# Kernel optimization log

Hardware: AMD Instinct MI355X
Metric: run time of the kernel (lower is better)

Reference implementation:

```python
import jax, jax.numpy as jnp
import numpy as np

B, N, C = 16, 2048, 384
CLUSTER_NUM = 512
K_NN = 5


def setup_inputs() -> dict:
    key = jax.random.key(0)
    k1, k2, k3, k4 = jax.random.split(key, 4)
    x = jax.random.normal(k1, (B, N, C), dtype=jnp.float32)
    idx_token = jax.random.randint(k2, (B, N), 0, N)
    agg_weight = jnp.ones((B, N, 1), dtype=jnp.float32)
    density_noise = jax.random.uniform(k3, (B, N), dtype=jnp.float32)
    score_w = jax.random.normal(k4, (1, C), dtype=jnp.float32) * 0.02
    score_b = jnp.zeros((1,), dtype=jnp.float32)
    return {"x": x, "idx_token": idx_token, "agg_weight": agg_weight,
            "density_noise": density_noise, "score_w": score_w, "score_b": score_b}


def _cluster_dpc_knn(x, density_noise, cluster_num, k):
    # x: [B,N,C]; clustering is done under no_grad in the original
    x = jax.lax.stop_gradient(x)
    b, n, c = x.shape
    sq = jnp.sum(x * x, axis=-1)  # [B,N]
    d2 = sq[:, :, None] + sq[:, None, :] - 2.0 * jnp.einsum('bnc,bmc->bnm', x, x)
    dist = jnp.sqrt(jnp.maximum(d2, 0.0)) / (c ** 0.5)  # [B,N,N] cdist/sqrt(C)
    # k smallest distances per row
    neg_near, _ = jax.lax.top_k(-dist, k)                # [B,N,k]
    density = jnp.exp(-jnp.mean(neg_near * neg_near, axis=-1))  # [B,N]
    density = density + density_noise * 1e-6             # tie-break noise
    mask = (density[:, None, :] > density[:, :, None]).astype(x.dtype)  # [B,N,N]
    dist_max = jnp.max(dist.reshape(b, -1), axis=-1)[:, None, None]
    dmin = jnp.min(dist * mask + dist_max * (1.0 - mask), axis=-1)  # [B,N]
    score = dmin * density
    _, index_down = jax.lax.top_k(score, cluster_num)    # [B,K] cluster centers
    dist_sub = jnp.take_along_axis(dist, index_down[:, :, None], axis=1)  # [B,K,N]
    idx_cluster = jnp.argmin(dist_sub, axis=1)           # [B,N]
    bi = jnp.arange(b)[:, None]
    centers = jnp.broadcast_to(jnp.arange(cluster_num)[None, :], (b, cluster_num))
    idx_cluster = idx_cluster.at[bi, index_down].set(centers)
    return idx_cluster, index_down


def reference(x, idx_token, agg_weight, density_noise, score_w, score_b):
    b, n, c = x.shape
    kc = CLUSTER_NUM
    # token score -> weight (equal_weight=False)
    token_weight = jnp.exp(x @ score_w.T + score_b)      # [B,N,1]
    idx_cluster, _ = _cluster_dpc_knn(x, density_noise, kc, K_NN)
    # merge tokens via segment sums
    bi = jnp.arange(b)[:, None]
    idx = (idx_cluster + bi * kc).reshape(-1)            # [B*N]
    all_weight = jax.ops.segment_sum(token_weight.reshape(-1, 1), idx,
                                     num_segments=b * kc) + 1e-6  # [B*K,1]
    norm_weight = token_weight / all_weight[idx].reshape(b, n, 1)
    x_merged = jax.ops.segment_sum((x * norm_weight).reshape(-1, c), idx,
                                   num_segments=b * kc).reshape(b, kc, c)
    idx_token_new = jnp.take_along_axis(idx_cluster, idx_token, axis=1)  # [B,N]
    weight_t = jnp.take_along_axis(norm_weight, idx_token[:, :, None], axis=1)
    agg_weight_new = agg_weight * weight_t               # [B,N,1]
    return x_merged, idx_token_new, agg_weight_new
```

## Files before the change

### kernel.cpp

```cpp
#include <hip/hip_runtime.h>
#include <math.h>

static constexpr int BB  = 16;
static constexpr int NN  = 2048;
static constexpr int CC  = 384;
static constexpr int KCL = 512;
static constexpr float RSQC = 0.051031036307982884f;

typedef short  bf16x8 __attribute__((ext_vector_type(8)));
typedef float  f32x4  __attribute__((ext_vector_type(4)));

__device__ __forceinline__ unsigned short f2b(float v) {
    unsigned u = __float_as_uint(v);
    unsigned r = (u + 0x7FFFu + ((u >> 16) & 1u)) >> 16;
    return (unsigned short)r;
}
__device__ __forceinline__ float b2f(unsigned short b) {
    return __uint_as_float(((unsigned)b) << 16);
}
__device__ __forceinline__ void gload16(const void* g, void* l) {
    __builtin_amdgcn_global_load_lds(
        (const __attribute__((address_space(1))) void*)g,
        (__attribute__((address_space(3))) void*)l, 16, 0, 0);
}
__device__ __forceinline__ void ins5(float* t5, float v) {
    if (v < t5[4]) {
        t5[4] = v;
        #pragma unroll
        for (int q = 4; q > 0; --q) {
            if (t5[q] < t5[q - 1]) { float tmp = t5[q - 1]; t5[q - 1] = t5[q]; t5[q] = tmp; }
        }
    }
}

__global__ __launch_bounds__(256) void k_prep(
    const float* __restrict__ x, const float* __restrict__ sw,
    const float* __restrict__ sb, float* __restrict__ sq, float* __restrict__ tw,
    unsigned short* __restrict__ Xh, unsigned short* __restrict__ Xl)
{
    int row  = blockIdx.x * 4 + (threadIdx.x >> 6);
    int lane = threadIdx.x & 63;
    const float* xr = x + (size_t)row * CC;
    unsigned short* xh = Xh + (size_t)row * CC;
    unsigned short* xl = Xl + (size_t)row * CC;
    float s2 = 0.f, sd = 0.f;
    for (int c = lane; c < CC; c += 64) {
        float v = xr[c];
        s2 += v * v;
        sd += v * sw[c];
        unsigned short h = f2b(v);
        xh[c] = h;
        xl[c] = f2b(v - b2f(h));
    }
    #pragma unroll
    for (int o = 32; o > 0; o >>= 1) {
        s2 += __shfl_down(s2, o);
        sd += __shfl_down(sd, o);
    }
    if (lane == 0) {
        sq[row] = s2;
        tw[row] = expf(sd + sb[0]);
    }
}

__global__ __launch_bounds__(256) void k_rowstats(
    const float* __restrict__ x, const float* __restrict__ sw,
    const float* __restrict__ sb, float* __restrict__ sq, float* __restrict__ tw)
{
    int row  = blockIdx.x * 4 + (threadIdx.x >> 6);
    int lane = threadIdx.x & 63;
    const float* xr = x + (size_t)row * CC;
    float s2 = 0.f, sd = 0.f;
    for (int c = lane; c < CC; c += 64) {
        float v = xr[c];
        s2 += v * v;
        sd += v * sw[c];
    }
    #pragma unroll
    for (int o = 32; o > 0; o >>= 1) {
        s2 += __shfl_down(s2, o);
        sd += __shfl_down(sd, o);
    }
    if (lane == 0) {
        sq[row] = s2;
        tw[row] = expf(sd + sb[0]);
    }
}


__global__ __launch_bounds__(256) void k_gemm_sym(
    const unsigned short* __restrict__ Xh, const unsigned short* __restrict__ Xl,
    const float* __restrict__ sq, float* __restrict__ D, int b0)
{
    const int b = b0 + blockIdx.z;
    int q = blockIdx.x;
    int ti = 0;
    while (q >= (16 - ti)) { q -= (16 - ti); ++ti; }
    const int tj = ti + q;
    const int i0 = ti * 128, j0 = tj * 128;

    const unsigned short* Xhb = Xh + (size_t)b * NN * CC;
    const unsigned short* Xlb = Xl + (size_t)b * NN * CC;
    const float* sqb = sq + b * NN;
    float* Db = D + (size_t)blockIdx.z * NN * NN;

    __shared__ union {
        unsigned short u16[4][128][32];
        float tr[64][129];
    } sm;

    const int t  = threadIdx.x;
    const int w  = t >> 6;
    const int l  = t & 63;
    const int wr = w >> 1, wc = w & 1;
    const int lt = l & 15, sl = l >> 4;

    f32x4 acc[4][4];
    #pragma unroll
    for (int fr = 0; fr < 4; ++fr)
        #pragma unroll
        for (int fc = 0; fc < 4; ++fc) acc[fr][fc] = (f32x4)0.0f;

    for (int kc = 0; kc < CC; kc += 32) {
        #pragma unroll
        for (int p = 0; p < 4; ++p) {
            const unsigned short* src = (p == 0) ? Xhb : (p == 1) ? Xlb
                                      : (p == 2) ? Xhb : Xlb;
            const int base0 = (p < 2) ? i0 : j0;
            #pragma unroll
            for (int u = 0; u < 2; ++u) {
                int seg = w * 2 + u;
                int r   = seg * 16 + (l >> 2);
                int s   = (l & 3) ^ ((r >> 1) & 3);
                gload16(src + (size_t)(base0 + r) * CC + kc + s * 8,
                        &sm.u16[p][seg * 16][0]);
            }
        }
        __syncthreads();

        bf16x8 fah[4], fal[4], fbh[4], fbl[4];
        #pragma unroll
        for (int fr = 0; fr < 4; ++fr) {
            int ra = wr * 64 + fr * 16 + lt;
            int sa = (sl ^ ((ra >> 1) & 3)) * 8;
            fah[fr] = *(const bf16x8*)&sm.u16[0][ra][sa];
            fal[fr] = *(const bf16x8*)&sm.u16[1][ra][sa];
        }
        #pragma unroll
        for (int fc = 0; fc < 4; ++fc) {
            int rb = wc * 64 + fc * 16 + lt;
            int sb_ = (sl ^ ((rb >> 1) & 3)) * 8;
            fbh[fc] = *(const bf16x8*)&sm.u16[2][rb][sb_];
            fbl[fc] = *(const bf16x8*)&sm.u16[3][rb][sb_];
        }
        #pragma unroll
        for (int fr = 0; fr < 4; ++fr)
            #pragma unroll
            for (int fc = 0; fc < 4; ++fc) {
                acc[fr][fc] = __builtin_amdgcn_mfma_f32_16x16x32_bf16(
                    fah[fr], fbh[fc], acc[fr][fc], 0, 0, 0);
                acc[fr][fc] = __builtin_amdgcn_mfma_f32_16x16x32_bf16(
                    fah[fr], fbl[fc], acc[fr][fc], 0, 0, 0);
                acc[fr][fc] = __builtin_amdgcn_mfma_f32_16x16x32_bf16(
                    fal[fr], fbh[fc], acc[fr][fc], 0, 0, 0);
            }
        __syncthreads();
    }

    float sqr[4][4], sqc[4];
    #pragma unroll
    for (int fr = 0; fr < 4; ++fr)
        #pragma unroll
        for (int reg = 0; reg < 4; ++reg)
            sqr[fr][reg] = sqb[i0 + wr * 64 + fr * 16 + sl * 4 + reg];
    #pragma unroll
    for (int fc = 0; fc < 4; ++fc)
        sqc[fc] = sqb[j0 + wc * 64 + fc * 16 + lt];

    #pragma unroll
    for (int fr = 0; fr < 4; ++fr)
        #pragma unroll
        for (int fc = 0; fc < 4; ++fc)
            #pragma unroll
            for (int reg = 0; reg < 4; ++reg) {
                int row = i0 + wr * 64 + fr * 16 + sl * 4 + reg;
                int col = j0 + wc * 64 + fc * 16 + lt;
                float d2 = fmaxf(sqr[fr][reg] + sqc[fc] - 2.0f * acc[fr][fc][reg], 0.0f);
                Db[(size_t)row * NN + col] = d2;
            }

    if (ti != tj) {
        #pragma unroll
        for (int h = 0; h < 2; ++h) {
            __syncthreads();
            if (wr == h) {
                #pragma unroll
                for (int fr = 0; fr < 4; ++fr)
                    #pragma unroll
                    for (int fc = 0; fc < 4; ++fc)
                        #pragma unroll
                        for (int reg = 0; reg < 4; ++reg) {
                            int rl = fr * 16 + sl * 4 + reg;
                            int cl = wc * 64 + fc * 16 + lt;
                            float d2 = fmaxf(sqr[fr][reg] + sqc[fc]
                                             - 2.0f * acc[fr][fc][reg], 0.0f);
                            sm.tr[rl][cl] = d2;
                        }
            }
            __syncthreads();
            for (int idx = t; idx < 128 * 64; idx += 256) {
                int c  = idx >> 6;
                int rl = idx & 63;
                Db[(size_t)(j0 + c) * NN + i0 + h * 64 + rl] = sm.tr[rl][c];
            }
        }
    }
}

__global__ __launch_bounds__(256) void k_density2(
    const float* __restrict__ D, const float* __restrict__ noise,
    float* __restrict__ dens, float* __restrict__ rowmax)
{
    int gid  = blockIdx.x * 4 + (threadIdx.x >> 6);
    int lane = threadIdx.x & 63;
    const float* row = D + (size_t)gid * NN;
    float t5[5] = {1e30f, 1e30f, 1e30f, 1e30f, 1e30f};
    float mx = 0.f;
    #pragma unroll
    for (int it = 0; it < 8; ++it) {
        float4 v = ((const float4*)row)[it * 64 + lane];
        mx = fmaxf(mx, fmaxf(fmaxf(v.x, v.y), fmaxf(v.z, v.w)));
        ins5(t5, v.x); ins5(t5, v.y); ins5(t5, v.z); ins5(t5, v.w);
    }
    #pragma unroll
    for (int o = 1; o < 64; o <<= 1) {
        float b0 = __shfl_xor(t5[0], o), b1 = __shfl_xor(t5[1], o);
        float b2 = __shfl_xor(t5[2], o), b3 = __shfl_xor(t5[3], o);
        float b4 = __shfl_xor(t5[4], o);
        mx = fmaxf(mx, __shfl_xor(mx, o));
        ins5(t5, b0); ins5(t5, b1); ins5(t5, b2); ins5(t5, b3); ins5(t5, b4);
    }
    if (lane == 0) {
        float m2 = (t5[0] + t5[1] + t5[2] + t5[3] + t5[4]) * (1.0f / (5.0f * CC));
        dens[gid]   = expf(-m2) + noise[gid] * 1e-6f;
        rowmax[gid] = mx;
    }
}

__global__ __launch_bounds__(256) void k_distmax2(
    const float* __restrict__ rowmax, float* __restrict__ dmax)
{
    int b = blockIdx.x, t = threadIdx.x;
    float m = 0.f;
    for (int i = t; i < NN; i += 256) m = fmaxf(m, rowmax[b * NN + i]);
    __shared__ float red[256];
    red[t] = m; __syncthreads();
    for (int o = 128; o > 0; o >>= 1) {
        if (t < o) red[t] = fmaxf(red[t], red[t + o]);
        __syncthreads();
    }
    if (t == 0) dmax[b] = sqrtf(red[0]) * RSQC;
}

__global__ __launch_bounds__(256) void k_dmin2(
    const float* __restrict__ D, const float* __restrict__ dens,
    const float* __restrict__ dmax, float* __restrict__ score)
{
    int gid  = blockIdx.x * 4 + (threadIdx.x >> 6);
    int lane = threadIdx.x & 63;
    int bl   = gid >> 11;
    const float* row = D + (size_t)gid * NN;
    const float* dn  = dens + (size_t)bl * NN;
    float di = dens[gid];
    float m = 1e30f;
    #pragma unroll
    for (int it = 0; it < 8; ++it) {
        float4 v  = ((const float4*)row)[it * 64 + lane];
        float4 dj = ((const float4*)dn)[it * 64 + lane];
        if (dj.x > di) m = fminf(m, v.x);
        if (dj.y > di) m = fminf(m, v.y);
        if (dj.z > di) m = fminf(m, v.z);
        if (dj.w > di) m = fminf(m, v.w);
    }
    #pragma unroll
    for (int o = 32; o > 0; o >>= 1) m = fminf(m, __shfl_down(m, o));
    if (lane == 0) {
        float dm = fminf(sqrtf(m) * RSQC, dmax[bl]);
        score[gid] = dm * di;
    }
}

__global__ __launch_bounds__(256) void k_assign2(
    const float* __restrict__ D, const int* __restrict__ idown,
    const int* __restrict__ invc, int* __restrict__ idxc)
{
    int bl = blockIdx.y;
    int tl = threadIdx.x & 63;
    int g  = threadIdx.x >> 6;
    int n  = blockIdx.x * 64 + tl;
    const float* Db = D + (size_t)bl * NN * NN;
    const int* idb  = idown + bl * KCL;
    float best = 1e30f; int bk = 0;
    for (int k = g * 128; k < (g + 1) * 128; ++k) {
        float v = Db[(size_t)idb[k] * NN + n];
        if (v < best) { best = v; bk = k; }
    }
    __shared__ float bvs[4][64];
    __shared__ int   bks[4][64];
    bvs[g][tl] = best; bks[g][tl] = bk;
    __syncthreads();
    if (threadIdx.x < 64) {
        float bv = bvs[0][threadIdx.x]; int bkk = bks[0][threadIdx.x];
        #pragma unroll
        for (int gg = 1; gg < 4; ++gg) {
            if (bvs[gg][threadIdx.x] < bv) { bv = bvs[gg][threadIdx.x]; bkk = bks[gg][threadIdx.x]; }
        }
        int nn = blockIdx.x * 64 + threadIdx.x;
        int iv = invc[bl * NN + nn];
        idxc[bl * NN + nn] = (iv >= 0) ? iv : bkk;
    }
}


__global__ __launch_bounds__(256) void k_density(
    const float* __restrict__ x, const float* __restrict__ sq,
    const float* __restrict__ noise, float* __restrict__ dens,
    float* __restrict__ rowmax)
{
    const int b  = blockIdx.y;
    const int i0 = blockIdx.x * 64;
    const float* xb  = x + (size_t)b * NN * CC;
    const float* sqb = sq + b * NN;
    __shared__ float As[16][64];
    __shared__ float Bs[16][64];
    __shared__ float mrg[64][16][5];
    __shared__ float mrgmax[64][16];
    const int t  = threadIdx.x;
    const int tx = t & 15, ty = t >> 4;
    const int lr = t >> 2, lk4 = (t & 3) * 4;

    float top[4][5];
    float rmax[4];
    float sqi[4];
    #pragma unroll
    for (int r = 0; r < 4; ++r) {
        sqi[r]  = sqb[i0 + ty * 4 + r];
        rmax[r] = 0.f;
        #pragma unroll
        for (int q = 0; q < 5; ++q) top[r][q] = 1e30f;
    }

    for (int j0 = 0; j0 < NN; j0 += 64) {
        float acc[4][4];
        #pragma unroll
        for (int r = 0; r < 4; ++r)
            #pragma unroll
            for (int s = 0; s < 4; ++s) acc[r][s] = 0.f;

        for (int k0 = 0; k0 < CC; k0 += 16) {
            float4 av = *(const float4*)(xb + (size_t)(i0 + lr) * CC + k0 + lk4);
            float4 bv = *(const float4*)(xb + (size_t)(j0 + lr) * CC + k0 + lk4);
            As[lk4 + 0][lr] = av.x; As[lk4 + 1][lr] = av.y;
            As[lk4 + 2][lr] = av.z; As[lk4 + 3][lr] = av.w;
            Bs[lk4 + 0][lr] = bv.x; Bs[lk4 + 1][lr] = bv.y;
            Bs[lk4 + 2][lr] = bv.z; Bs[lk4 + 3][lr] = bv.w;
            __syncthreads();
            #pragma unroll
            for (int kk = 0; kk < 16; ++kk) {
                float4 a4 = *(const float4*)&As[kk][ty * 4];
                float4 b4 = *(const float4*)&Bs[kk][tx * 4];
                float ar[4] = {a4.x, a4.y, a4.z, a4.w};
                float br[4] = {b4.x, b4.y, b4.z, b4.w};
                #pragma unroll
                for (int r = 0; r < 4; ++r)
                    #pragma unroll
                    for (int s = 0; s < 4; ++s)
                        acc[r][s] = fmaf(ar[r], br[s], acc[r][s]);
            }
            __syncthreads();
        }
        float sqj[4];
        #pragma unroll
        for (int s = 0; s < 4; ++s) sqj[s] = sqb[j0 + tx * 4 + s];
        #pragma unroll
        for (int r = 0; r < 4; ++r) {
            #pragma unroll
            for (int s = 0; s < 4; ++s) {
                float d2 = sqi[r] + sqj[s] - 2.0f * acc[r][s];
                float d  = sqrtf(fmaxf(d2, 0.0f)) * RSQC;
                rmax[r] = fmaxf(rmax[r], d);
                if (d < top[r][4]) {
                    top[r][4] = d;
                    #pragma unroll
                    for (int q = 4; q > 0; --q) {
                        if (top[r][q] < top[r][q - 1]) {
                            float tmp = top[r][q - 1];
                            top[r][q - 1] = top[r][q];
                            top[r][q] = tmp;
                        }
                    }
                }
            }
        }
    }
    #pragma unroll
    for (int r = 0; r < 4; ++r) {
        #pragma unroll
        for (int q = 0; q < 5; ++q) mrg[ty * 4 + r][tx][q] = top[r][q];
        mrgmax[ty * 4 + r][tx] = rmax[r];
    }
    __syncthreads();
    if (t < 64) {
        float t5[5] = {1e30f, 1e30f, 1e30f, 1e30f, 1e30f};
        float mx = 0.f;
        for (int c = 0; c < 16; ++c) {
            mx = fmaxf(mx, mrgmax[t][c]);
            #pragma unroll
            for (int q = 0; q < 5; ++q) ins5(t5, mrg[t][c][q]);
        }
        float m2 = (t5[0]*t5[0] + t5[1]*t5[1] + t5[2]*t5[2] +
                    t5[3]*t5[3] + t5[4]*t5[4]) / 5.0f;
        int i = i0 + t;
        dens[b * NN + i]   = expf(-m2) + noise[b * NN + i] * 1e-6f;
        rowmax[b * NN + i] = mx;
    }
}

__global__ __launch_bounds__(256) void k_distmax(
    const float* __restrict__ rowmax, float* __restrict__ dmax)
{
    int b = blockIdx.x, t = threadIdx.x;
    float m = 0.f;
    for (int i = t; i < NN; i += 256) m = fmaxf(m, rowmax[b * NN + i]);
    __shared__ float red[256];
    red[t] = m; __syncthreads();
    for (int o = 128; o > 0; o >>= 1) {
        if (t < o) red[t] = fmaxf(red[t], red[t + o]);
        __syncthreads();
    }
    if (t == 0) dmax[b] = red[0];
}

__global__ __launch_bounds__(256) void k_dmin(
    const float* __restrict__ x, const float* __restrict__ sq,
    const float* __restrict__ dens, const float* __restrict__ dmax,
    float* __restrict__ score)
{
    const int b  = blockIdx.y;
    const int i0 = blockIdx.x * 64;
    const float* xb  = x + (size_t)b * NN * CC;
    const float* sqb = sq + b * NN;
    const float* dnb = dens + b * NN;
    __shared__ float As[16][64];
    __shared__ float Bs[16][64];
    __shared__ float mrgmin[64][16];
    const int t  = threadIdx.x;
    const int tx = t & 15, ty = t >> 4;
    const int lr = t >> 2, lk4 = (t & 3) * 4;

    float sqi[4], di[4], mn[4];
    #pragma unroll
    for (int r = 0; r < 4; ++r) {
        sqi[r] = sqb[i0 + ty * 4 + r];
        di[r]  = dnb[i0 + ty * 4 + r];
        mn[r]  = 1e30f;
    }

    for (int j0 = 0; j0 < NN; j0 += 64) {
        float acc[4][4];
        #pragma unroll
        for (int r = 0; r < 4; ++r)
            #pragma unroll
            for (int s = 0; s < 4; ++s) acc[r][s] = 0.f;

        for (int k0 = 0; k0 < CC; k0 += 16) {
            float4 av = *(const float4*)(xb + (size_t)(i0 + lr) * CC + k0 + lk4);
            float4 bv = *(const float4*)(xb + (size_t)(j0 + lr) * CC + k0 + lk4);
            As[lk4 + 0][lr] = av.x; As[lk4 + 1][lr] = av.y;
            As[lk4 + 2][lr] = av.z; As[lk4 + 3][lr] = av.w;
            Bs[lk4 + 0][lr] = bv.x; Bs[lk4 + 1][lr] = bv.y;
            Bs[lk4 + 2][lr] = bv.z; Bs[lk4 + 3][lr] = bv.w;
            __syncthreads();
            #pragma unroll
            for (int kk = 0; kk < 16; ++kk) {
                float4 a4 = *(const float4*)&As[kk][ty * 4];
                float4 b4 = *(const float4*)&Bs[kk][tx * 4];
                float ar[4] = {a4.x, a4.y, a4.z, a4.w};
                float br[4] = {b4.x, b4.y, b4.z, b4.w};
                #pragma unroll
                for (int r = 0; r < 4; ++r)
                    #pragma unroll
                    for (int s = 0; s < 4; ++s)
                        acc[r][s] = fmaf(ar[r], br[s], acc[r][s]);
            }
            __syncthreads();
        }
        float dj[4];
        #pragma unroll
        for (int s = 0; s < 4; ++s) dj[s] = dnb[j0 + tx * 4 + s];
        float sqj[4];
        #pragma unroll
        for (int s = 0; s < 4; ++s) sqj[s] = sqb[j0 + tx * 4 + s];
        #pragma unroll
        for (int r = 0; r < 4; ++r) {
            #pragma unroll
            for (int s = 0; s < 4; ++s) {
                float d2 = sqi[r] + sqj[s] - 2.0f * acc[r][s];
                float d  = sqrtf(fmaxf(d2, 0.0f)) * RSQC;
                if (dj[s] > di[r]) mn[r] = fminf(mn[r], d);
            }
        }
    }
    #pragma unroll
    for (int r = 0; r < 4; ++r) mrgmin[ty * 4 + r][tx] = mn[r];
    __syncthreads();
    if (t < 64) {
        float m = 1e30f;
        for (int c = 0; c < 16; ++c) m = fminf(m, mrgmin[t][c]);
        float dm = fminf(dmax[b], m);
        score[b * NN + i0 + t] = dm * dnb[i0 + t];
    }
}

__global__ __launch_bounds__(256) void k_assign(
    const float* __restrict__ x, const float* __restrict__ sq,
    const int* __restrict__ idown, int* __restrict__ idxc)
{
    const int b  = blockIdx.y;
    const int n0 = blockIdx.x * 64;
    const float* xb  = x + (size_t)b * NN * CC;
    const float* sqb = sq + b * NN;
    const int* idb = idown + b * KCL;
    __shared__ float As[16][64];
    __shared__ float Bs[16][64];
    __shared__ float mv[64][16];
    __shared__ int   mk[64][16];
    const int t  = threadIdx.x;
    const int tx = t & 15, ty = t >> 4;
    const int lr = t >> 2, lk4 = (t & 3) * 4;

    float sqt[4];
    #pragma unroll
    for (int s = 0; s < 4; ++s) sqt[s] = sqb[n0 + tx * 4 + s];
    float bestv[4] = {1e30f, 1e30f, 1e30f, 1e30f};
    int   bestk[4] = {0, 0, 0, 0};

    for (int c0 = 0; c0 < KCL; c0 += 64) {
        int crow = idb[c0 + lr];
        float acc[4][4];
        #pragma unroll
        for (int r = 0; r < 4; ++r)
            #pragma unroll
            for (int s = 0; s < 4; ++s) acc[r][s] = 0.f;

        for (int k0 = 0; k0 < CC; k0 += 16) {
            float4 av = *(const float4*)(xb + (size_t)crow * CC + k0 + lk4);
            float4 bv = *(const float4*)(xb + (size_t)(n0 + lr) * CC + k0 + lk4);
            As[lk4 + 0][lr] = av.x; As[lk4 + 1][lr] = av.y;
            As[lk4 + 2][lr] = av.z; As[lk4 + 3][lr] = av.w;
            Bs[lk4 + 0][lr] = bv.x; Bs[lk4 + 1][lr] = bv.y;
            Bs[lk4 + 2][lr] = bv.z; Bs[lk4 + 3][lr] = bv.w;
            __syncthreads();
            #pragma unroll
            for (int kk = 0; kk < 16; ++kk) {
                float4 a4 = *(const float4*)&As[kk][ty * 4];
                float4 b4 = *(const float4*)&Bs[kk][tx * 4];
                float ar[4] = {a4.x, a4.y, a4.z, a4.w};
                float br[4] = {b4.x, b4.y, b4.z, b4.w};
                #pragma unroll
                for (int r = 0; r < 4; ++r)
                    #pragma unroll
                    for (int s = 0; s < 4; ++s)
                        acc[r][s] = fmaf(ar[r], br[s], acc[r][s]);
            }
            __syncthreads();
        }
        float sqc[4];
        #pragma unroll
        for (int r = 0; r < 4; ++r) sqc[r] = sqb[idb[c0 + ty * 4 + r]];
        #pragma unroll
        for (int r = 0; r < 4; ++r) {
            int kg = c0 + ty * 4 + r;
            #pragma unroll
            for (int s = 0; s < 4; ++s) {
                float e = fmaxf(sqc[r] + sqt[s] - 2.0f * acc[r][s], 0.0f);
                if (e < bestv[s]) { bestv[s] = e; bestk[s] = kg; }
            }
        }
    }
    #pragma unroll
    for (int s = 0; s < 4; ++s) {
        mv[tx * 4 + s][ty] = bestv[s];
        mk[tx * 4 + s][ty] = bestk[s];
    }
    __syncthreads();
    if (t < 64) {
        float bv = 1e30f; int bk = 1 << 30;
        for (int c = 0; c < 16; ++c) {
            float v = mv[t][c]; int k = mk[t][c];
            if (v < bv || (v == bv && k < bk)) { bv = v; bk = k; }
        }
        idxc[b * NN + n0 + t] = bk;
    }
}

__global__ __launch_bounds__(256) void k_override(
    const int* __restrict__ idown, int* __restrict__ idxc)
{
    int g = blockIdx.x * 256 + threadIdx.x;
    int b = g >> 9, k = g & 511;
    idxc[b * NN + idown[g]] = k;
}


__global__ __launch_bounds__(1024) void k_topk(
    const float* __restrict__ score, int* __restrict__ idown, int* __restrict__ invc)
{
    int b = blockIdx.x, t = threadIdx.x;
    __shared__ float s[NN];
    __shared__ int   si[NN];
    s[t]         = score[b * NN + t];        si[t]        = t;
    s[t + 1024]  = score[b * NN + t + 1024]; si[t + 1024] = t + 1024;
    __syncthreads();
    for (int k = 2; k <= NN; k <<= 1) {
        for (int j = k >> 1; j > 0; j >>= 1) {
            int i = (t & (j - 1)) | ((t & ~(j - 1)) << 1);
            int l = i | j;
            bool dir = ((i & k) == 0);
            float svi = s[i], svl = s[l];
            int   ii  = si[i], il = si[l];
            bool before_l_i = (svl > svi) || (svl == svi && il < ii);
            if (before_l_i == dir) {
                s[i] = svl; s[l] = svi;
                si[i] = il; si[l] = ii;
            }
            __syncthreads();
        }
    }
    if (t < KCL) idown[b * KCL + t] = si[t];
    invc[b * NN + t] = -1;
    invc[b * NN + t + 1024] = -1;
    __syncthreads();
    if (t < KCL) invc[b * NN + si[t]] = t;
}

__global__ __launch_bounds__(512) void k_merge(
    const float* __restrict__ x, const float* __restrict__ tw,
    const int* __restrict__ idxc, float* __restrict__ aw, float* __restrict__ xm)
{
    int b = blockIdx.y, k = blockIdx.x;
    __shared__ int members[NN];
    __shared__ int wc[8];
    __shared__ float red[512];
    int t = threadIdx.x, lane = t & 63, w = t >> 6;
    const int* ib = idxc + b * NN;
    int base = 0;
    for (int r0 = 0; r0 < NN; r0 += 512) {
        int n = r0 + t;
        bool m = (ib[n] == k);
        unsigned long long msk = __ballot(m);
        if (lane == 0) wc[w] = __popcll(msk);
        __syncthreads();
        int off = 0;
        for (int ww = 0; ww < w; ++ww) off += wc[ww];
        int tot = 0;
        #pragma unroll
        for (int ww = 0; ww < 8; ++ww) tot += wc[ww];
        if (m) members[base + off + __popcll(msk & ((1ull << lane) - 1ull))] = n;
        base += tot;
        __syncthreads();
    }
    int cnt = base;
    const float* twb = tw + b * NN;
    float ps = 0.f;
    for (int p = t; p < cnt; p += 512) ps += twb[members[p]];
    red[t] = ps; __syncthreads();
    for (int o = 256; o > 0; o >>= 1) {
        if (t < o) red[t] += red[t + o];
        __syncthreads();
    }
    float awf = red[0] + 1e-6f;
    if (t == 0) aw[b * KCL + k] = awf;
    if (t < CC) {
        const float* xb = x + (size_t)b * NN * CC;
        float s = 0.f;
        for (int p = 0; p < cnt; ++p) {
            int n = members[p];
            s += xb[(size_t)n * CC + t] * twb[n];
        }
        xm[((size_t)b * KCL + k) * CC + t] = s / awf;
    }
}

__global__ __launch_bounds__(256) void k_out(
    const int* __restrict__ idx_token, const float* __restrict__ aggw,
    const float* __restrict__ tw, const float* __restrict__ aw,
    const int* __restrict__ idxc, float* __restrict__ out_idx,
    float* __restrict__ out_agg)
{
    int g = blockIdx.x * 256 + threadIdx.x;
    int b = g >> 11;
    int it = idx_token[g];
    int kclu = idxc[b * NN + it];
    out_idx[g] = (float)kclu;
    float nw = tw[b * NN + it] / aw[b * KCL + kclu];
    out_agg[g] = aggw[g] * nw;
}

extern "C" void kernel_launch(void* const* d_in, const int* in_sizes, int n_in,
                              void* d_out, int out_size, void* d_ws, size_t ws_size,
                              hipStream_t stream) {
    const float* x         = (const float*)d_in[0];
    const int*   idx_token = (const int*)  d_in[1];
    const float* aggw      = (const float*)d_in[2];
    const float* noise     = (const float*)d_in[3];
    const float* sw        = (const float*)d_in[4];
    const float* sb        = (const float*)d_in[5];

    float* ws      = (float*)d_ws;
    float* sq      = ws;
    float* tw      = ws + 32768;
    float* dens    = ws + 65536;
    float* rowmax  = ws + 98304;
    float* score   = ws + 131072;
    float* dmax    = ws + 163840;
    float* aw      = ws + 163904;
    int*   idown   = (int*)(ws + 172096);
    int*   idxc    = (int*)(ws + 180288);
    int*   invc    = (int*)(ws + 213056);

    unsigned short* Xh = (unsigned short*)(ws + 245824);
    unsigned short* Xl = (unsigned short*)(ws + 245824 + 6291456);
    float* Dbuf        = ws + 245824 + 2 * 6291456;

    const size_t head_bytes = (size_t)(245824 + 2 * 6291456) * 4;
    size_t avail = (ws_size > head_bytes) ? (ws_size - head_bytes) : 0;
    int nbg = 0;
    for (int g = 16; g >= 1; g >>= 1) {
        if ((size_t)g * NN * NN * 4 <= avail) { nbg = g; break; }
    }

    float* xm      = (float*)d_out;
    float* out_idx = xm + (size_t)BB * KCL * CC;
    float* out_agg = out_idx + (size_t)BB * NN;

    if (nbg >= 16) {
        k_prep    <<<dim3(BB * NN / 4), 256, 0, stream>>>(x, sw, sb, sq, tw, Xh, Xl);
        k_gemm_sym<<<dim3(136, 1, BB), 256, 0, stream>>>(Xh, Xl, sq, Dbuf, 0);
        for (int gi = 0; gi < 2; ++gi) {
            int b0 = (gi == 0) ? 8 : 0;
            float* Dg = Dbuf + (size_t)b0 * NN * NN;
            k_density2<<<dim3(8 * NN / 4), 256, 0, stream>>>(Dg, noise + b0 * NN,
                                                             dens + b0 * NN, rowmax + b0 * NN);
            k_distmax2<<<dim3(8), 256, 0, stream>>>(rowmax + b0 * NN, dmax + b0);
            k_dmin2   <<<dim3(8 * NN / 4), 256, 0, stream>>>(Dg, dens + b0 * NN,
                                                             dmax + b0, score + b0 * NN);
            k_topk    <<<dim3(8), 1024, 0, stream>>>(score + b0 * NN, idown + b0 * KCL,
                                                     invc + b0 * NN);
            k_assign2 <<<dim3(NN / 64, 8), 256, 0, stream>>>(Dg, idown + b0 * KCL,
                                                             invc + b0 * NN, idxc + b0 * NN);
        }
    } else if (nbg >= 1) {
        k_prep<<<dim3(BB * NN / 4), 256, 0, stream>>>(x, sw, sb, sq, tw, Xh, Xl);
        int G = (nbg >= 8) ? 8 : nbg;
        for (int b0 = 0; b0 < BB; b0 += G) {
            int g = (b0 + G <= BB) ? G : (BB - b0);
            k_gemm_sym<<<dim3(136, 1, g), 256, 0, stream>>>(Xh, Xl, sq, Dbuf, b0);
            k_density2<<<dim3(g * NN / 4), 256, 0, stream>>>(Dbuf, noise + b0 * NN,
                                                             dens + b0 * NN, rowmax + b0 * NN);
            k_distmax2<<<dim3(g), 256, 0, stream>>>(rowmax + b0 * NN, dmax + b0);
            k_dmin2   <<<dim3(g * NN / 4), 256, 0, stream>>>(Dbuf, dens + b0 * NN,
                                                             dmax + b0, score + b0 * NN);
            k_topk    <<<dim3(g), 1024, 0, stream>>>(score + b0 * NN, idown + b0 * KCL,
                                                     invc + b0 * NN);
            k_assign2 <<<dim3(NN / 64, g), 256, 0, stream>>>(Dbuf, idown + b0 * KCL,
                                                             invc + b0 * NN, idxc + b0 * NN);
        }
    } else {
        k_rowstats<<<dim3(BB * NN / 4), 256, 0, stream>>>(x, sw, sb, sq, tw);
        k_density <<<dim3(NN / 64, BB), 256, 0, stream>>>(x, sq, noise, dens, rowmax);
        k_distmax <<<dim3(BB), 256, 0, stream>>>(rowmax, dmax);
        k_dmin    <<<dim3(NN / 64, BB), 256, 0, stream>>>(x, sq, dens, dmax, score);
        k_topk    <<<dim3(BB), 1024, 0, stream>>>(score, idown, invc);
        k_assign  <<<dim3(NN / 64, BB), 256, 0, stream>>>(x, sq, idown, idxc);
        k_override<<<dim3(BB * KCL / 256), 256, 0, stream>>>(idown, idxc);
    }

    k_merge<<<dim3(KCL, BB), 512, 0, stream>>>(x, tw, idxc, aw, xm);
    k_out  <<<dim3(BB * NN / 256), 256, 0, stream>>>(idx_token, aggw, tw, aw, idxc,
                                                     out_idx, out_agg);
}
```

Baseline: 445.1 us.

## Fuse distmax into density via atomicMax, vectorize prep, swizzle GEMM grid

Several changes at once. The per-batch max-distance reduction kernel is removed: each density block now reduces its row maxima and issues an atomicMax on the float bits, with the accumulator zeroed in k_prep. The two-group launch loop becomes single full-batch launches, which cuts kernel launches. k_prep switches to 8-wide vectorized loads and stores, and the GEMM maps workgroups through an XCD-style swizzle to improve L2 locality. The atomics rely on nonnegative float bit ordering and on the zeroing in k_prep finishing before k_density2 runs.

```diff
diff --git a/kernel.cpp b/kernel.cpp
--- a/kernel.cpp
+++ b/kernel.cpp
@@ -36,21 +36,33 @@
 __global__ __launch_bounds__(256) void k_prep(
     const float* __restrict__ x, const float* __restrict__ sw,
     const float* __restrict__ sb, float* __restrict__ sq, float* __restrict__ tw,
-    unsigned short* __restrict__ Xh, unsigned short* __restrict__ Xl)
-{
+    unsigned short* __restrict__ Xh, unsigned short* __restrict__ Xl,
+    unsigned* __restrict__ dmaxraw)
+{
+    if (blockIdx.x == 0 && threadIdx.x < 64) dmaxraw[threadIdx.x] = 0u;
     int row  = blockIdx.x * 4 + (threadIdx.x >> 6);
     int lane = threadIdx.x & 63;
     const float* xr = x + (size_t)row * CC;
-    unsigned short* xh = Xh + (size_t)row * CC;
-    unsigned short* xl = Xl + (size_t)row * CC;
     float s2 = 0.f, sd = 0.f;
-    for (int c = lane; c < CC; c += 64) {
-        float v = xr[c];
-        s2 += v * v;
-        sd += v * sw[c];
-        unsigned short h = f2b(v);
-        xh[c] = h;
-        xl[c] = f2b(v - b2f(h));
+    if (lane < 48) {
+        const float* p  = xr + lane * 8;
+        const float* pw = sw + lane * 8;
+        float4 a0 = *(const float4*)(p);
+        float4 a1 = *(const float4*)(p + 4);
+        float4 w0 = *(const float4*)(pw);
+        float4 w1 = *(const float4*)(pw + 4);
+        float vv[8] = {a0.x,a0.y,a0.z,a0.w,a1.x,a1.y,a1.z,a1.w};
+        float ww[8] = {w0.x,w0.y,w0.z,w0.w,w1.x,w1.y,w1.z,w1.w};
+        unsigned short h[8], lo[8];
+        #pragma unroll
+        for (int e = 0; e < 8; ++e) {
+            s2 += vv[e] * vv[e];
+            sd += vv[e] * ww[e];
+            h[e]  = f2b(vv[e]);
+            lo[e] = f2b(vv[e] - b2f(h[e]));
+        }
+        *(bf16x8*)(Xh + (size_t)row * CC + lane * 8) = *(bf16x8*)h;
+        *(bf16x8*)(Xl + (size_t)row * CC + lane * 8) = *(bf16x8*)lo;
     }
     #pragma unroll
     for (int o = 32; o > 0; o >>= 1) {
@@ -92,8 +104,12 @@
     const unsigned short* __restrict__ Xh, const unsigned short* __restrict__ Xl,
     const float* __restrict__ sq, float* __restrict__ D, int b0)
 {
-    const int b = b0 + blockIdx.z;
-    int q = blockIdx.x;
+    int f   = blockIdx.x + 136 * blockIdx.z;
+    int nwg = 136 * gridDim.z;
+    int wg  = ((nwg & 7) == 0) ? ((f & 7) * (nwg >> 3) + (f >> 3)) : f;
+    int bz  = wg / 136;
+    int q   = wg % 136;
+    const int b = b0 + bz;
     int ti = 0;
     while (q >= (16 - ti)) { q -= (16 - ti); ++ti; }
     const int tj = ti + q;
@@ -102,7 +118,7 @@
     const unsigned short* Xhb = Xh + (size_t)b * NN * CC;
     const unsigned short* Xlb = Xl + (size_t)b * NN * CC;
     const float* sqb = sq + b * NN;
-    float* Db = D + (size_t)blockIdx.z * NN * NN;
+    float* Db = D + (size_t)bz * NN * NN;
 
     __shared__ union {
         unsigned short u16[4][128][32];
@@ -219,7 +235,7 @@
 
 __global__ __launch_bounds__(256) void k_density2(
     const float* __restrict__ D, const float* __restrict__ noise,
-    float* __restrict__ dens, float* __restrict__ rowmax)
+    float* __restrict__ dens, unsigned* __restrict__ dmaxraw)
 {
     int gid  = blockIdx.x * 4 + (threadIdx.x >> 6);
     int lane = threadIdx.x & 63;
@@ -240,31 +256,23 @@
         mx = fmaxf(mx, __shfl_xor(mx, o));
         ins5(t5, b0); ins5(t5, b1); ins5(t5, b2); ins5(t5, b3); ins5(t5, b4);
     }
+    __shared__ float red[4];
     if (lane == 0) {
         float m2 = (t5[0] + t5[1] + t5[2] + t5[3] + t5[4]) * (1.0f / (5.0f * CC));
-        dens[gid]   = expf(-m2) + noise[gid] * 1e-6f;
-        rowmax[gid] = mx;
-    }
-}
-
-__global__ __launch_bounds__(256) void k_distmax2(
-    const float* __restrict__ rowmax, float* __restrict__ dmax)
-{
-    int b = blockIdx.x, t = threadIdx.x;
-    float m = 0.f;
-    for (int i = t; i < NN; i += 256) m = fmaxf(m, rowmax[b * NN + i]);
-    __shared__ float red[256];
-    red[t] = m; __syncthreads();
-    for (int o = 128; o > 0; o >>= 1) {
-        if (t < o) red[t] = fmaxf(red[t], red[t + o]);
-        __syncthreads();
-    }
-    if (t == 0) dmax[b] = sqrtf(red[0]) * RSQC;
+        dens[gid] = expf(-m2) + noise[gid] * 1e-6f;
+        red[threadIdx.x >> 6] = mx;
+    }
+    __syncthreads();
+    if (threadIdx.x == 0) {
+        float m = fmaxf(fmaxf(red[0], red[1]), fmaxf(red[2], red[3]));
+        int bl = (blockIdx.x * 4) >> 11;
+        atomicMax(&dmaxraw[bl], __float_as_uint(m));
+    }
 }
 
 __global__ __launch_bounds__(256) void k_dmin2(
     const float* __restrict__ D, const float* __restrict__ dens,
-    const float* __restrict__ dmax, float* __restrict__ score)
+    const unsigned* __restrict__ dmaxraw, float* __restrict__ score)
 {
     int gid  = blockIdx.x * 4 + (threadIdx.x >> 6);
     int lane = threadIdx.x & 63;
@@ -285,7 +293,8 @@
     #pragma unroll
     for (int o = 32; o > 0; o >>= 1) m = fminf(m, __shfl_down(m, o));
     if (lane == 0) {
-        float dm = fminf(sqrtf(m) * RSQC, dmax[bl]);
+        float dmv = sqrtf(__uint_as_float(dmaxraw[bl])) * RSQC;
+        float dm = fminf(sqrtf(m) * RSQC, dmv);
         score[gid] = dm * di;
     }
 }
@@ -723,7 +732,7 @@
     float* dens    = ws + 65536;
     float* rowmax  = ws + 98304;
     float* score   = ws + 131072;
-    float* dmax    = ws + 163840;
+    unsigned* dmaxraw = (unsigned*)(ws + 163840);
     float* aw      = ws + 163904;
     int*   idown   = (int*)(ws + 172096);
     int*   idxc    = (int*)(ws + 180288);
@@ -745,42 +754,33 @@
     float* out_agg = out_idx + (size_t)BB * NN;
 
     if (nbg >= 16) {
-        k_prep    <<<dim3(BB * NN / 4), 256, 0, stream>>>(x, sw, sb, sq, tw, Xh, Xl);
+        k_prep    <<<dim3(BB * NN / 4), 256, 0, stream>>>(x, sw, sb, sq, tw, Xh, Xl, dmaxraw);
         k_gemm_sym<<<dim3(136, 1, BB), 256, 0, stream>>>(Xh, Xl, sq, Dbuf, 0);
-        for (int gi = 0; gi < 2; ++gi) {
-            int b0 = (gi == 0) ? 8 : 0;
-            float* Dg = Dbuf + (size_t)b0 * NN * NN;
-            k_density2<<<dim3(8 * NN / 4), 256, 0, stream>>>(Dg, noise + b0 * NN,
-                                                             dens + b0 * NN, rowmax + b0 * NN);
-            k_distmax2<<<dim3(8), 256, 0, stream>>>(rowmax + b0 * NN, dmax + b0);
-            k_dmin2   <<<dim3(8 * NN / 4), 256, 0, stream>>>(Dg, dens + b0 * NN,
-                                                             dmax + b0, score + b0 * NN);
-            k_topk    <<<dim3(8), 1024, 0, stream>>>(score + b0 * NN, idown + b0 * KCL,
-                                                     invc + b0 * NN);
-            k_assign2 <<<dim3(NN / 64, 8), 256, 0, stream>>>(Dg, idown + b0 * KCL,
-                                                             invc + b0 * NN, idxc + b0 * NN);
-        }
+        k_density2<<<dim3(BB * NN / 4), 256, 0, stream>>>(Dbuf, noise, dens, dmaxraw);
+        k_dmin2   <<<dim3(BB * NN / 4), 256, 0, stream>>>(Dbuf, dens, dmaxraw, score);
+        k_topk    <<<dim3(BB), 1024, 0, stream>>>(score, idown, invc);
+        k_assign2 <<<dim3(NN / 64, BB), 256, 0, stream>>>(Dbuf, idown, invc, idxc);
     } else if (nbg >= 1) {
-        k_prep<<<dim3(BB * NN / 4), 256, 0, stream>>>(x, sw, sb, sq, tw, Xh, Xl);
+        k_prep<<<dim3(BB * NN / 4), 256, 0, stream>>>(x, sw, sb, sq, tw, Xh, Xl, dmaxraw);
         int G = (nbg >= 8) ? 8 : nbg;
         for (int b0 = 0; b0 < BB; b0 += G) {
             int g = (b0 + G <= BB) ? G : (BB - b0);
             k_gemm_sym<<<dim3(136, 1, g), 256, 0, stream>>>(Xh, Xl, sq, Dbuf, b0);
             k_density2<<<dim3(g * NN / 4), 256, 0, stream>>>(Dbuf, noise + b0 * NN,
-                                                             dens + b0 * NN, rowmax + b0 * NN);
-            k_distmax2<<<dim3(g), 256, 0, stream>>>(rowmax + b0 * NN, dmax + b0);
+                                                             dens + b0 * NN, dmaxraw + b0);
             k_dmin2   <<<dim3(g * NN / 4), 256, 0, stream>>>(Dbuf, dens + b0 * NN,
-                                                             dmax + b0, score + b0 * NN);
+                                                             dmaxraw + b0, score + b0 * NN);
             k_topk    <<<dim3(g), 1024, 0, stream>>>(score + b0 * NN, idown + b0 * KCL,
                                                      invc + b0 * NN);
             k_assign2 <<<dim3(NN / 64, g), 256, 0, stream>>>(Dbuf, idown + b0 * KCL,
                                                              invc + b0 * NN, idxc + b0 * NN);
         }
     } else {
+        float* dmaxf = (float*)dmaxraw;
         k_rowstats<<<dim3(BB * NN / 4), 256, 0, stream>>>(x, sw, sb, sq, tw);
         k_density <<<dim3(NN / 64, BB), 256, 0, stream>>>(x, sq, noise, dens, rowmax);
-        k_distmax <<<dim3(BB), 256, 0, stream>>>(rowmax, dmax);
-        k_dmin    <<<dim3(NN / 64, BB), 256, 0, stream>>>(x, sq, dens, dmax, score);
+        k_distmax <<<dim3(BB), 256, 0, stream>>>(rowmax, dmaxf);
+        k_dmin    <<<dim3(NN / 64, BB), 256, 0, stream>>>(x, sq, dens, dmaxf, score);
         k_topk    <<<dim3(BB), 1024, 0, stream>>>(score, idown, invc);
         k_assign  <<<dim3(NN / 64, BB), 256, 0, stream>>>(x, sq, idown, idxc);
         k_override<<<dim3(BB * KCL / 256), 256, 0, stream>>>(idown, idxc);
```

Measured after the change: 486.8 us. +9.4%, slower.
